# Kernel optimization log

Hardware: AMD Instinct MI355X
Metric: run time of the kernel (lower is better)

The kernel has to match this reference:

```python
import jax, jax.numpy as jnp
import numpy as np

N_HITS = 16384
N_EDGES = 262144
N_GROUPS = 512
N_EVENTS = 64
IN_CH = 25
HID = 128
HEADS = 4
DH = HID // HEADS
LAYERS = 3
EDGE_DIM = 5
FFN = 4 * HID
EPS = 1e-5


def setup_inputs() -> dict:
    key = jax.random.key(0)
    ks = jax.random.split(key, 16)
    def nrm(k, shape, s=0.05):
        return jax.random.normal(k, shape, dtype=jnp.float32) * s
    z = lambda *s: jnp.zeros(s, jnp.float32)
    return {
        "x": jax.random.normal(ks[0], (N_HITS, IN_CH), dtype=jnp.float32),
        "edge_index": jax.random.randint(ks[1], (2, N_EDGES), 0, N_HITS, dtype=jnp.int32),
        "edge_attr": jax.random.normal(ks[2], (N_EDGES, EDGE_DIM), dtype=jnp.float32),
        "group_indices": jax.random.randint(ks[3], (N_HITS,), 0, N_GROUPS, dtype=jnp.int32),
        "batch_indices_per_group": jnp.sort(jax.random.randint(ks[4], (N_GROUPS,), 0, N_EVENTS, dtype=jnp.int32)),
        "embed_W": nrm(ks[5], (IN_CH, HID)),
        "embed_b": z(HID),
        "blk_Wqkv": nrm(ks[6], (LAYERS, HID, 3 * HID)),
        "blk_bqkv": z(LAYERS, 3 * HID),
        "blk_We": nrm(ks[7], (LAYERS, EDGE_DIM, HID)),
        "blk_be": z(LAYERS, HID),
        "blk_Wo": nrm(ks[8], (LAYERS, HID, HID)),
        "blk_bo": z(LAYERS, HID),
        "ln1_g": jnp.ones((LAYERS, HID), jnp.float32),
        "ln1_b": z(LAYERS, HID),
        "ffn_W1": nrm(ks[9], (LAYERS, HID, FFN)),
        "ffn_b1": z(LAYERS, FFN),
        "ffn_W2": nrm(ks[10], (LAYERS, FFN, HID)),
        "ffn_b2": z(LAYERS, HID),
        "ln2_g": jnp.ones((LAYERS, HID), jnp.float32),
        "ln2_b": z(LAYERS, HID),
        "aff_W1": nrm(ks[11], (4 * HID, HID)),
        "aff_b1": z(HID),
        "aff_W2": nrm(ks[12], (HID, 1)),
        "aff_b2": z(1),
    }


def _layer_norm(v, g, b):
    mu = jnp.mean(v, axis=-1, keepdims=True)
    var = jnp.mean((v - mu) ** 2, axis=-1, keepdims=True)
    return (v - mu) * jax.lax.rsqrt(var + EPS) * g + b


def reference(x, edge_index, edge_attr, group_indices, batch_indices_per_group,
              embed_W, embed_b, blk_Wqkv, blk_bqkv, blk_We, blk_be, blk_Wo, blk_bo,
              ln1_g, ln1_b, ffn_W1, ffn_b1, ffn_W2, ffn_b2, ln2_g, ln2_b,
              aff_W1, aff_b1, aff_W2, aff_b2):
    n = x.shape[0]
    G = batch_indices_per_group.shape[0]
    src, dst = edge_index[0], edge_index[1]
    scale = 1.0 / np.sqrt(DH).astype(np.float32)

    h = x @ embed_W + embed_b  # [N, HID]
    for l in range(LAYERS):
        # edge-conditioned multi-head attention over the graph edges
        qkv = h @ blk_Wqkv[l] + blk_bqkv[l]
        q, k, v = jnp.split(qkv, 3, axis=-1)
        e = edge_attr @ blk_We[l] + blk_be[l]          # [E, HID]
        qe = q[dst].reshape(-1, HEADS, DH)              # [E, h, d]
        ke = (k[src] + e).reshape(-1, HEADS, DH)
        ve = (v[src] + e).reshape(-1, HEADS, DH)
        logits = jnp.einsum("ehd,ehd->eh", qe, ke) * scale
        m = jax.ops.segment_max(logits, dst, num_segments=n)
        m = jnp.where(jnp.isfinite(m), m, 0.0)          # nodes with no in-edges
        p = jnp.exp(logits - m[dst])
        s = jax.ops.segment_sum(p, dst, num_segments=n)
        attn = jax.ops.segment_sum(p[:, :, None] * ve, dst, num_segments=n)
        attn = (attn / jnp.maximum(s, 1e-9)[:, :, None]).reshape(n, HID)
        h = _layer_norm(h + attn @ blk_Wo[l] + blk_bo[l], ln1_g[l], ln1_b[l])
        f = jax.nn.relu(h @ ffn_W1[l] + ffn_b1[l]) @ ffn_W2[l] + ffn_b2[l]
        h = _layer_norm(h + f, ln2_g[l], ln2_b[l])

    # group pooling (multi-scatter)
    raw_view = x[:, 3].astype(jnp.int32)  # truncation, matches torch .long()
    cnt_all = jax.ops.segment_sum(jnp.ones((n,), jnp.float32), group_indices, num_segments=G)
    g_max = jax.ops.segment_max(h, group_indices, num_segments=G)
    g_max = jnp.where(cnt_all[:, None] > 0, g_max, 0.0)  # torch_scatter fills empty with 0

    def pool_view(view_id):
        w = (raw_view == view_id).astype(jnp.float32)
        cnt = jax.ops.segment_sum(w, group_indices, num_segments=G)
        summ = jax.ops.segment_sum(h * w[:, None], group_indices, num_segments=G)
        pooled = summ / jnp.maximum(cnt, 1.0)[:, None]
        has = (cnt > 0).astype(jnp.float32)[:, None]
        return pooled, has

    pool_x, has_x = pool_view(0)
    pool_y, has_y = pool_view(1)
    sum_feat = pool_x * has_x + pool_y * has_y
    valid = jnp.maximum(has_x + has_y, 1.0)
    ge = jnp.concatenate([sum_feat / valid, g_max], axis=1)  # [G, 2*HID]

    # pairwise affinity MLP: Linear(4H->H) split so the [G,G,4H] concat is never built
    W1a, W1b = aff_W1[: 2 * HID], aff_W1[2 * HID:]
    pre = (ge @ W1a)[:, None, :] + (ge @ W1b)[None, :, :] + aff_b1  # [G, G, HID]
    scores = (jax.nn.relu(pre) @ aff_W2 + aff_b2)[..., 0]           # [G, G]
    scores = 0.5 * (scores + scores.T)
    event_mask = batch_indices_per_group[:, None] == batch_indices_per_group[None, :]
    return jax.nn.sigmoid(scores) * event_mask.astype(scores.dtype)
```

## Files before the change

kernel.cpp:

```cpp
#include <hip/hip_runtime.h>
#include <hip/hip_bf16.h>

#define NHITS   16384
#define NEDGES  262144
#define NGROUPS 512
#define HID     128
#define LAYERS  3
#define FFND    512
#define MAXDEG  64
#define GCAP    96

typedef __attribute__((ext_vector_type(8))) short bf16x8;
typedef __attribute__((ext_vector_type(8))) unsigned short ushort8;
typedef __attribute__((ext_vector_type(4))) float floatx4;

__device__ __forceinline__ float bf2f(ushort u) {
    return __uint_as_float(((unsigned)u) << 16);
}
__device__ __forceinline__ ushort f2bf(float f) {
    unsigned u = __float_as_uint(f);
    unsigned r = (u + 0x7FFFu + ((u >> 16) & 1u)) >> 16;
    return (ushort)r;
}

__device__ __forceinline__ void gl2lds16(const ushort* gp, ushort* lp) {
    __builtin_amdgcn_global_load_lds(
        (const __attribute__((address_space(1))) unsigned int*)(gp),
        (__attribute__((address_space(3))) unsigned int*)(lp), 16, 0, 0);
}


struct TD { const float* src; ushort* dst; int K; int N; };
struct TDs { TD d[14]; };

__global__ __launch_bounds__(256) void transpose_all(TDs tds, int* __restrict__ zbuf,
                                                     int ztotal) {
    __shared__ float lds[32][33];
    if (blockIdx.y == 0) {
        for (int gz = blockIdx.x * 256 + threadIdx.x; gz < ztotal; gz += 64 * 256)
            zbuf[gz] = 0;
    }
    TD d = tds.d[blockIdx.y];
    int tX = d.N >> 5;
    int tiles = (d.K >> 5) * tX;
    if ((int)blockIdx.x >= tiles) return;
    int tk = blockIdx.x / tX, tn = blockIdx.x % tX;
    int k0 = tk * 32, n0 = tn * 32;
    int r = threadIdx.x >> 5, c = threadIdx.x & 31;
#pragma unroll
    for (int i = 0; i < 4; ++i)
        lds[r + i * 8][c] = d.src[(size_t)(k0 + r + i * 8) * d.N + n0 + c];
    __syncthreads();
#pragma unroll
    for (int i = 0; i < 4; ++i) {
        int n = n0 + r + i * 8;
        d.dst[(size_t)n * d.K + k0 + c] = f2bf(lds[c][r + i * 8]);
    }
}


__global__ __launch_bounds__(256) void scatter_embed(
        const int* __restrict__ src, const int* __restrict__ dst,
        const float* __restrict__ ea, const int* __restrict__ gidx,
        int* __restrict__ cnt, int* __restrict__ cnt2,
        int* __restrict__ ps, float* __restrict__ pea, int* __restrict__ hlist,
        const float* __restrict__ x, const float* __restrict__ embW,
        const float* __restrict__ embB, float* __restrict__ h,
        ushort* __restrict__ hb) {
    const int vb = blockIdx.x, t = threadIdx.x;
    if (vb < 1024) {
        int e = vb * 256 + t;
        int d = dst[e];
        int slot = atomicAdd(&cnt[d], 1);
        if (slot < MAXDEG) {
            size_t pos = (size_t)d * MAXDEG + slot;
            ps[pos] = src[e];
#pragma unroll
            for (int j = 0; j < 5; ++j) pea[pos * 5 + j] = ea[(size_t)e * 5 + j];
        }
        if (e < NHITS) {
            int g = gidx[e];
            int slot2 = atomicAdd(&cnt2[g], 1);
            if (slot2 < GCAP) hlist[g * GCAP + slot2] = e;
        }
    } else {
        __shared__ float xs[2][32];
        int base = (vb - 1024) * 32;
        for (int it = 0; it < 16; ++it) {
            int i0 = base + it * 2;
            __syncthreads();
            if (t < 25) xs[0][t] = x[(size_t)i0 * 25 + t];
            else if (t >= 128 && t < 153) xs[1][t - 128] = x[(size_t)(i0 + 1) * 25 + (t - 128)];
            __syncthreads();
            int node = i0 + (t >> 7), c = t & 127;
            const float* xr = xs[t >> 7];
            float s = embB[c];
#pragma unroll
            for (int k = 0; k < 25; ++k) s += xr[k] * embW[k * HID + c];
            h[(size_t)node * HID + c] = s;
            hb[(size_t)node * HID + c] = f2bf(s);
        }
    }
}


__global__ __launch_bounds__(256) void gemm_mfma_k(const ushort* __restrict__ A,
                                                   const ushort* __restrict__ Bt,
                                                   const float* __restrict__ bias,
                                                   ushort* __restrict__ C,
                                                   int N, int K, int relu) {
    __shared__ ushort As[128 * 32];
    __shared__ ushort Bs[128 * 32];
    const int t = threadIdx.x;
    const int lane = t & 63;
    const int w = t >> 6;
    const int wr = w >> 1, wc = w & 1;
    const int lm = lane & 15, q = lane >> 4;
    const int row0 = blockIdx.y * 128;
    const int col0 = blockIdx.x * 128;
    const int sr = t >> 2, sc = (t & 3) * 8;
    const int sr2 = (t + 256) >> 2, sc2 = ((t + 256) & 3) * 8;

    floatx4 acc[4][4] = {};
    for (int k0 = 0; k0 < K; k0 += 32) {
        gl2lds16(A + (size_t)(row0 + sr) * K + k0 + sc,   &As[t * 8]);
        gl2lds16(A + (size_t)(row0 + sr2) * K + k0 + sc2, &As[t * 8 + 2048]);
        gl2lds16(Bt + (size_t)(col0 + sr) * K + k0 + sc,   &Bs[t * 8]);
        gl2lds16(Bt + (size_t)(col0 + sr2) * K + k0 + sc2, &Bs[t * 8 + 2048]);
        __syncthreads();
        bf16x8 af[4], bf[4];
#pragma unroll
        for (int it = 0; it < 4; ++it)
            af[it] = *(const bf16x8*)&As[(wr * 64 + it * 16 + lm) * 32 + q * 8];
#pragma unroll
        for (int jt = 0; jt < 4; ++jt)
            bf[jt] = *(const bf16x8*)&Bs[(wc * 64 + jt * 16 + lm) * 32 + q * 8];
#pragma unroll
        for (int it = 0; it < 4; ++it)
#pragma unroll
            for (int jt = 0; jt < 4; ++jt)
                acc[it][jt] = __builtin_amdgcn_mfma_f32_16x16x32_bf16(
                    af[it], bf[jt], acc[it][jt], 0, 0, 0);
        __syncthreads();
    }
#pragma unroll
    for (int jt = 0; jt < 4; ++jt) {
        int col = col0 + wc * 64 + jt * 16 + lm;
        float bb = bias ? bias[col] : 0.f;
#pragma unroll
        for (int it = 0; it < 4; ++it)
#pragma unroll
            for (int r = 0; r < 4; ++r) {
                int row = row0 + wr * 64 + it * 16 + q * 4 + r;
                float o = acc[it][jt][r] + bb;
                if (relu) o = fmaxf(o, 0.f);
                C[(size_t)row * N + col] = f2bf(o);
            }
    }
}


__global__ __launch_bounds__(256) void gemm_qkv_k(const ushort* __restrict__ A,
                                                  const ushort* __restrict__ Bt,
                                                  const float* __restrict__ bias,
                                                  ushort* __restrict__ qb,
                                                  ushort* __restrict__ kvb,
                                                  int K) {
    __shared__ ushort As[128 * 32];
    __shared__ ushort Bs[128 * 32];
    const int t = threadIdx.x;
    const int lane = t & 63;
    const int w = t >> 6;
    const int wr = w >> 1, wc = w & 1;
    const int lm = lane & 15, q = lane >> 4;
    const int row0 = blockIdx.y * 128;
    const int col0 = blockIdx.x * 128;
    const int sr = t >> 2, sc = (t & 3) * 8;
    const int sr2 = (t + 256) >> 2, sc2 = ((t + 256) & 3) * 8;

    floatx4 acc[4][4] = {};
    for (int k0 = 0; k0 < K; k0 += 32) {
        gl2lds16(A + (size_t)(row0 + sr) * K + k0 + sc,   &As[t * 8]);
        gl2lds16(A + (size_t)(row0 + sr2) * K + k0 + sc2, &As[t * 8 + 2048]);
        gl2lds16(Bt + (size_t)(col0 + sr) * K + k0 + sc,   &Bs[t * 8]);
        gl2lds16(Bt + (size_t)(col0 + sr2) * K + k0 + sc2, &Bs[t * 8 + 2048]);
        __syncthreads();
        bf16x8 af[4], bf[4];
#pragma unroll
        for (int it = 0; it < 4; ++it)
            af[it] = *(const bf16x8*)&As[(wr * 64 + it * 16 + lm) * 32 + q * 8];
#pragma unroll
        for (int jt = 0; jt < 4; ++jt)
            bf[jt] = *(const bf16x8*)&Bs[(wc * 64 + jt * 16 + lm) * 32 + q * 8];
#pragma unroll
        for (int it = 0; it < 4; ++it)
#pragma unroll
            for (int jt = 0; jt < 4; ++jt)
                acc[it][jt] = __builtin_amdgcn_mfma_f32_16x16x32_bf16(
                    af[it], bf[jt], acc[it][jt], 0, 0, 0);
        __syncthreads();
    }
#pragma unroll
    for (int jt = 0; jt < 4; ++jt) {
        int col = col0 + wc * 64 + jt * 16 + lm;
        float bb = bias[col];
#pragma unroll
        for (int it = 0; it < 4; ++it)
#pragma unroll
            for (int r = 0; r < 4; ++r) {
                int row = row0 + wr * 64 + it * 16 + q * 4 + r;
                float o = acc[it][jt][r] + bb;
                ushort ob = f2bf(o);
                if (col < 128) qb[(size_t)row * 128 + col] = ob;
                else           kvb[(size_t)row * 256 + (col - 128)] = ob;
            }
    }
}


__global__ __launch_bounds__(256) void attn_kernel(const ushort* __restrict__ qb,
                                                   const ushort* __restrict__ kvb,
                                                   const int* __restrict__ ps,
                                                   const float* __restrict__ pea,
                                                   const int* __restrict__ cnt,
                                                   const float* __restrict__ We,
                                                   const float* __restrict__ be,
                                                   ushort* __restrict__ attnb) {
    __shared__ float WeS[640], beS[128];
    int t = threadIdx.x;
    for (int idx = t; idx < 640; idx += 256) WeS[idx] = We[idx];
    if (t < 128) beS[t] = be[t];
    __syncthreads();
    const int i = blockIdx.x * 4 + (t >> 6);
    const int lane = t & 63;
    const int grp = lane >> 4;
    const int cb = (lane & 15) * 8;
    float qv[8];
    {
        ushort8 qq = *(const ushort8*)(qb + (size_t)i * 128 + cb);
#pragma unroll
        for (int j = 0; j < 8; ++j) qv[j] = bf2f(qq[j]);
    }
    float pj[6];
#pragma unroll
    for (int k = 0; k < 5; ++k) {
        float s = 0.f;
#pragma unroll
        for (int j = 0; j < 8; ++j) s += qv[j] * WeS[k * 128 + cb + j];
        pj[k] = s;
    }
    {
        float sb = 0.f;
#pragma unroll
        for (int j = 0; j < 8; ++j) sb += qv[j] * beS[cb + j];
        pj[5] = sb;
    }
#pragma unroll
    for (int k = 0; k < 6; ++k) {
        pj[k] += __shfl_xor(pj[k], 1);
        pj[k] += __shfl_xor(pj[k], 2);
    }
    float S = 0.f, T0 = 0.f, T1 = 0.f, T2 = 0.f, T3 = 0.f, T4 = 0.f;
    float acc[8] = {};
    const int endc = min(cnt[i], MAXDEG);
    const size_t pbase = (size_t)i * MAXDEG;
    const float scale = 0.17677669529663687f;

#pragma unroll 4
    for (int p0 = 0; p0 < endc; p0 += 4) {
        int pp = p0 + grp;
        bool act = pp < endc;
        int slot = act ? pp : (endc - 1);
        int s = ps[pbase + slot];
        const float* eap = pea + (pbase + slot) * 5;
        float a0 = eap[0], a1 = eap[1], a2 = eap[2], a3 = eap[3], a4 = eap[4];
        const ushort* srow = kvb + (size_t)s * 256;
        ushort8 kk = *(const ushort8*)(srow + cb);
        ushort8 vv = *(const ushort8*)(srow + 128 + cb);
        float part = 0.f;
#pragma unroll
        for (int j = 0; j < 8; ++j) part += qv[j] * bf2f(kk[j]);
        part += __shfl_xor(part, 1);
        part += __shfl_xor(part, 2);
        float logit = (part + pj[5] + a0 * pj[0] + a1 * pj[1] + a2 * pj[2]
                       + a3 * pj[3] + a4 * pj[4]) * scale;
        float pe = act ? __expf(logit) : 0.f;
        S += pe;
        T0 += pe * a0; T1 += pe * a1; T2 += pe * a2; T3 += pe * a3; T4 += pe * a4;
#pragma unroll
        for (int j = 0; j < 8; ++j) acc[j] += pe * bf2f(vv[j]);
    }
#pragma unroll
    for (int j = 0; j < 8; ++j) {
        acc[j] += __shfl_xor(acc[j], 16);
        acc[j] += __shfl_xor(acc[j], 32);
    }
    S += __shfl_xor(S, 16);   S += __shfl_xor(S, 32);
    T0 += __shfl_xor(T0, 16); T0 += __shfl_xor(T0, 32);
    T1 += __shfl_xor(T1, 16); T1 += __shfl_xor(T1, 32);
    T2 += __shfl_xor(T2, 16); T2 += __shfl_xor(T2, 32);
    T3 += __shfl_xor(T3, 16); T3 += __shfl_xor(T3, 32);
    T4 += __shfl_xor(T4, 16); T4 += __shfl_xor(T4, 32);
    if (grp == 0) {
        float inv = 1.f / fmaxf(S, 1e-9f);
        ushort8 o;
#pragma unroll
        for (int j = 0; j < 8; ++j) {
            float wadd = WeS[cb + j] * T0 + WeS[128 + cb + j] * T1
                       + WeS[256 + cb + j] * T2 + WeS[384 + cb + j] * T3
                       + WeS[512 + cb + j] * T4 + beS[cb + j] * S;
            o[j] = f2bf((acc[j] + wadd) * inv);
        }
        *(ushort8*)(attnb + (size_t)i * HID + cb) = o;
    }
}


__global__ __launch_bounds__(256) void woffn_k(
        const ushort* __restrict__ attnb,
        const ushort* __restrict__ Wot, const float* __restrict__ bo,
        const float* __restrict__ ln1g, const float* __restrict__ ln1b,
        const ushort* __restrict__ W1t, const float* __restrict__ b1v,
        const ushort* __restrict__ W2t, const float* __restrict__ b2v,
        const float* __restrict__ ln2g, const float* __restrict__ ln2b,
        float* __restrict__ h, ushort* __restrict__ hb) {
    __shared__ ushort As[32 * 136];
    __shared__ ushort Bs[128 * 32];
    __shared__ ushort mid[32 * 520];
    __shared__ float redS[64], redQ[64];
    const int t = threadIdx.x;
    const int lane = t & 63;
    const int w = t >> 6;
    const int wr = w >> 1, wc = w & 1;
    const int lm = lane & 15, q = lane >> 4;
    const int row0 = blockIdx.x * 32;
    const int sr = t >> 2, sc = (t & 3) * 8;
    const int sr2 = (t + 256) >> 2, sc2 = ((t + 256) & 3) * 8;

    for (int i = t; i < 32 * 16; i += 256) {
        int row = i >> 4, c8 = (i & 15) * 8;
        *(ushort8*)&As[row * 136 + c8] =
            *(const ushort8*)(attnb + (size_t)(row0 + row) * HID + c8);
    }
    __syncthreads();

    floatx4 accW[4] = {};
    for (int k0 = 0; k0 < 128; k0 += 32) {
        gl2lds16(Wot + (size_t)sr * HID + k0 + sc,   &Bs[t * 8]);
        gl2lds16(Wot + (size_t)sr2 * HID + k0 + sc2, &Bs[t * 8 + 2048]);
        __syncthreads();
        bf16x8 af = *(const bf16x8*)&As[(wr * 16 + lm) * 136 + k0 + q * 8];
#pragma unroll
        for (int jt = 0; jt < 4; ++jt) {
            bf16x8 bf = *(const bf16x8*)&Bs[(wc * 64 + jt * 16 + lm) * 32 + q * 8];
            accW[jt] = __builtin_amdgcn_mfma_f32_16x16x32_bf16(af, bf, accW[jt], 0, 0, 0);
        }
        __syncthreads();
    }
    float o1[4][4];
    {
        float psum[4] = {}, psq[4] = {};
#pragma unroll
        for (int jt = 0; jt < 4; ++jt) {
            int col = wc * 64 + jt * 16 + lm;
            float bb = bo[col];
#pragma unroll
            for (int r = 0; r < 4; ++r) {
                int row = row0 + wr * 16 + q * 4 + r;
                float v = accW[jt][r] + bb + h[(size_t)row * HID + col];
                o1[jt][r] = v;
                psum[r] += v;
                psq[r] += v * v;
            }
        }
#pragma unroll
        for (int r = 0; r < 4; ++r) {
            float s = psum[r], ss = psq[r];
#pragma unroll
            for (int k = 1; k < 16; k <<= 1) {
                s += __shfl_xor(s, k, 16);
                ss += __shfl_xor(ss, k, 16);
            }
            psum[r] = s; psq[r] = ss;
        }
        if (lm == 0)
#pragma unroll
            for (int r = 0; r < 4; ++r) {
                int rl = wr * 16 + q * 4 + r;
                redS[rl * 2 + wc] = psum[r];
                redQ[rl * 2 + wc] = psq[r];
            }
        __syncthreads();
#pragma unroll
        for (int r = 0; r < 4; ++r) {
            int rl = wr * 16 + q * 4 + r;
            float tot = redS[rl * 2] + redS[rl * 2 + 1];
            float totq = redQ[rl * 2] + redQ[rl * 2 + 1];
            float mu = tot * (1.f / HID);
            float var = totq * (1.f / HID) - mu * mu;
            float rstd = rsqrtf(var + 1e-5f);
#pragma unroll
            for (int jt = 0; jt < 4; ++jt) {
                int col = wc * 64 + jt * 16 + lm;
                float o = (o1[jt][r] - mu) * rstd * ln1g[col] + ln1b[col];
                o1[jt][r] = o;
                As[(wr * 16 + q * 4 + r) * 136 + col] = f2bf(o);
            }
        }
    }
    __syncthreads();

    for (int nc = 0; nc < 4; ++nc) {
        floatx4 acc1[4] = {};
        for (int k0 = 0; k0 < 128; k0 += 32) {
            gl2lds16(W1t + (size_t)(nc * 128 + sr) * HID + k0 + sc,   &Bs[t * 8]);
            gl2lds16(W1t + (size_t)(nc * 128 + sr2) * HID + k0 + sc2, &Bs[t * 8 + 2048]);
            __syncthreads();
            bf16x8 af = *(const bf16x8*)&As[(wr * 16 + lm) * 136 + k0 + q * 8];
#pragma unroll
            for (int jt = 0; jt < 4; ++jt) {
                bf16x8 bf = *(const bf16x8*)&Bs[(wc * 64 + jt * 16 + lm) * 32 + q * 8];
                acc1[jt] = __builtin_amdgcn_mfma_f32_16x16x32_bf16(af, bf, acc1[jt], 0, 0, 0);
            }
            __syncthreads();
        }
#pragma unroll
        for (int jt = 0; jt < 4; ++jt) {
            int col = wc * 64 + jt * 16 + lm;
            float bb = b1v[nc * 128 + col];
#pragma unroll
            for (int r = 0; r < 4; ++r) {
                int row = wr * 16 + q * 4 + r;
                mid[row * 520 + nc * 128 + col] = f2bf(fmaxf(acc1[jt][r] + bb, 0.f));
            }
        }
    }
    __syncthreads();

    floatx4 acc2[4] = {};
    for (int k0 = 0; k0 < 512; k0 += 32) {
        gl2lds16(W2t + (size_t)sr * FFND + k0 + sc,   &Bs[t * 8]);
        gl2lds16(W2t + (size_t)sr2 * FFND + k0 + sc2, &Bs[t * 8 + 2048]);
        __syncthreads();
        bf16x8 af = *(const bf16x8*)&mid[(wr * 16 + lm) * 520 + k0 + q * 8];
#pragma unroll
        for (int jt = 0; jt < 4; ++jt) {
            bf16x8 bf = *(const bf16x8*)&Bs[(wc * 64 + jt * 16 + lm) * 32 + q * 8];
            acc2[jt] = __builtin_amdgcn_mfma_f32_16x16x32_bf16(af, bf, acc2[jt], 0, 0, 0);
        }
        __syncthreads();
    }
    float psum[4] = {}, psq[4] = {};
#pragma unroll
    for (int jt = 0; jt < 4; ++jt) {
        int col = wc * 64 + jt * 16 + lm;
        float bb = b2v[col];
#pragma unroll
        for (int r = 0; r < 4; ++r) {
            float v = acc2[jt][r] + bb + o1[jt][r];
            acc2[jt][r] = v;
            psum[r] += v;
            psq[r] += v * v;
        }
    }
#pragma unroll
    for (int r = 0; r < 4; ++r) {
        float s = psum[r], ss = psq[r];
#pragma unroll
        for (int k = 1; k < 16; k <<= 1) {
            s += __shfl_xor(s, k, 16);
            ss += __shfl_xor(ss, k, 16);
        }
        psum[r] = s; psq[r] = ss;
    }
    if (lm == 0)
#pragma unroll
        for (int r = 0; r < 4; ++r) {
            int rl = wr * 16 + q * 4 + r;
            redS[rl * 2 + wc] = psum[r];
            redQ[rl * 2 + wc] = psq[r];
        }
    __syncthreads();
#pragma unroll
    for (int r = 0; r < 4; ++r) {
        int rl = wr * 16 + q * 4 + r;
        float tot = redS[rl * 2] + redS[rl * 2 + 1];
        float totq = redQ[rl * 2] + redQ[rl * 2 + 1];
        float mu = tot * (1.f / HID);
        float var = totq * (1.f / HID) - mu * mu;
        float rstd = rsqrtf(var + 1e-5f);
        int row = row0 + rl;
#pragma unroll
        for (int jt = 0; jt < 4; ++jt) {
            int col = wc * 64 + jt * 16 + lm;
            float o = (acc2[jt][r] - mu) * rstd * ln2g[col] + ln2b[col];
            h[(size_t)row * HID + col] = o;
            hb[(size_t)row * HID + col] = f2bf(o);
        }
    }
}


__global__ __launch_bounds__(128) void pool_group(const float* __restrict__ h,
                                                  const float* __restrict__ x,
                                                  const int* __restrict__ hlist,
                                                  const int* __restrict__ cnt2,
                                                  ushort* __restrict__ geb) {
    int g = blockIdx.x, c = threadIdx.x;
    int n = min(cnt2[g], GCAP);
    float mx = -INFINITY, sx = 0.f, sy = 0.f, cx = 0.f, cy = 0.f;
    for (int p = 0; p < n; ++p) {
        int i = hlist[g * GCAP + p];
        float hv = h[(size_t)i * HID + c];
        mx = fmaxf(mx, hv);
        int view = (int)x[(size_t)i * 25 + 3];
        if (view == 0) { sx += hv; cx += 1.f; }
        else if (view == 1) { sy += hv; cy += 1.f; }
    }
    float gm = (n > 0) ? mx : 0.f;
    float px = sx / fmaxf(cx, 1.f), py = sy / fmaxf(cy, 1.f);
    float hx = cx > 0.f ? 1.f : 0.f, hy = cy > 0.f ? 1.f : 0.f;
    float sf = px * hx + py * hy;
    float valid = fmaxf(hx + hy, 1.f);
    geb[g * 256 + c] = f2bf(sf / valid);
    geb[g * 256 + 128 + c] = f2bf(gm);
}


__global__ __launch_bounds__(256) void score_final(const ushort* __restrict__ Cab,
                                                   const float* __restrict__ W2,
                                                   const float* __restrict__ b1v,
                                                   const float* __restrict__ b2,
                                                   const int* __restrict__ ev,
                                                   float* __restrict__ out) {
    int bi = blockIdx.y, bj = blockIdx.x;
    if (bj < bi) return;
    __shared__ float Ai[16][129], Bi[16][129], Aj[16][129], Bj[16][129];
    __shared__ float w2s[128], b1s[128];
    int t = threadIdx.y * 16 + threadIdx.x;
    int i0 = bi * 16, j0 = bj * 16;
    for (int idx = t; idx < 2048; idx += 256) {
        int r = idx >> 7, k = idx & 127;
        Ai[r][k] = bf2f(Cab[(size_t)(i0 + r) * 256 + k]);
        Bi[r][k] = bf2f(Cab[(size_t)(i0 + r) * 256 + 128 + k]);
        Aj[r][k] = bf2f(Cab[(size_t)(j0 + r) * 256 + k]);
        Bj[r][k] = bf2f(Cab[(size_t)(j0 + r) * 256 + 128 + k]);
    }
    if (t < 128) { w2s[t] = W2[t]; b1s[t] = b1v[t]; }
    __syncthreads();
    int tx = threadIdx.x, ty = threadIdx.y;
    float sij = 0.f, sji = 0.f;
#pragma unroll 4
    for (int k = 0; k < 128; ++k) {
        float pb = b1s[k], wk = w2s[k];
        sij += fmaxf(Ai[ty][k] + Bj[tx][k] + pb, 0.f) * wk;
        sji += fmaxf(Aj[tx][k] + Bi[ty][k] + pb, 0.f) * wk;
    }
    float z = 0.5f * (sij + sji) + b2[0];
    float sg = 1.f / (1.f + __expf(-z));
    int gi = i0 + ty, gj = j0 + tx;
    float res = (ev[gi] == ev[gj]) ? sg : 0.f;
    out[(size_t)gi * NGROUPS + gj] = res;
    out[(size_t)gj * NGROUPS + gi] = res;
}


static inline char* align256(char* p) {
    return (char*)(((uintptr_t)p + 255) & ~(uintptr_t)255);
}

extern "C" void kernel_launch(void* const* d_in, const int* in_sizes, int n_in,
                              void* d_out, int out_size, void* d_ws, size_t ws_size,
                              hipStream_t stream) {
    const float* x    = (const float*)d_in[0];
    const int* eidx   = (const int*)d_in[1];
    const float* ea   = (const float*)d_in[2];
    const int* gidx   = (const int*)d_in[3];
    const int* ev     = (const int*)d_in[4];
    const float* embW = (const float*)d_in[5];
    const float* embB = (const float*)d_in[6];
    const float* Wqkv = (const float*)d_in[7];
    const float* bqkv = (const float*)d_in[8];
    const float* We   = (const float*)d_in[9];
    const float* be   = (const float*)d_in[10];
    const float* Wo   = (const float*)d_in[11];
    const float* bo   = (const float*)d_in[12];
    const float* ln1g = (const float*)d_in[13];
    const float* ln1b = (const float*)d_in[14];
    const float* W1   = (const float*)d_in[15];
    const float* b1   = (const float*)d_in[16];
    const float* W2   = (const float*)d_in[17];
    const float* b2   = (const float*)d_in[18];
    const float* ln2g = (const float*)d_in[19];
    const float* ln2b = (const float*)d_in[20];
    const float* affW1 = (const float*)d_in[21];
    const float* affb1 = (const float*)d_in[22];
    const float* affW2 = (const float*)d_in[23];
    const float* affb2 = (const float*)d_in[24];

    const int* src = eidx;
    const int* dst = eidx + NEDGES;

    char* p = (char*)d_ws;
    float* h    = (float*)p;            p += (size_t)NHITS * HID * 4;
    float* pea  = (float*)p;            p += (size_t)NHITS * MAXDEG * 5 * 4;
    int* cnt    = (int*)p;              p += NHITS * 4;
    int* cnt2   = (int*)p;              p += NGROUPS * 4;
    int* ps     = (int*)p;              p += (size_t)NHITS * MAXDEG * 4;
    int* hlist  = (int*)p;              p += NGROUPS * GCAP * 4;
    p = align256(p);
    ushort* hb    = (ushort*)p;         p += (size_t)NHITS * HID * 2;
    ushort* qb    = (ushort*)p;         p += (size_t)NHITS * 128 * 2;
    ushort* kvb   = (ushort*)p;         p += (size_t)NHITS * 256 * 2;
    ushort* attnb = (ushort*)p;         p += (size_t)NHITS * HID * 2;
    ushort* geb   = (ushort*)p;         p += (size_t)NGROUPS * 256 * 2;
    ushort* Cab   = (ushort*)p;         p += (size_t)NGROUPS * 256 * 2;
    p = align256(p);
    ushort* Wqkvt = (ushort*)p;         p += (size_t)LAYERS * 384 * HID * 2;
    ushort* Wot   = (ushort*)p;         p += (size_t)LAYERS * HID * HID * 2;
    ushort* W1t   = (ushort*)p;         p += (size_t)LAYERS * FFND * HID * 2;
    ushort* W2t   = (ushort*)p;         p += (size_t)LAYERS * HID * FFND * 2;
    ushort* W1abt = (ushort*)p;         p += (size_t)256 * 256 * 2;

    TDs tds;
    for (int l = 0; l < LAYERS; ++l) {
        tds.d[l * 4 + 0] = { Wqkv + (size_t)l * HID * 384, Wqkvt + (size_t)l * 384 * HID, HID, 384 };
        tds.d[l * 4 + 1] = { Wo + (size_t)l * HID * HID,   Wot + (size_t)l * HID * HID,   HID, HID };
        tds.d[l * 4 + 2] = { W1 + (size_t)l * HID * FFND,  W1t + (size_t)l * FFND * HID,  HID, FFND };
        tds.d[l * 4 + 3] = { W2 + (size_t)l * FFND * HID,  W2t + (size_t)l * HID * FFND,  FFND, HID };
    }
    tds.d[12] = { affW1,             W1abt,             256, HID };
    tds.d[13] = { affW1 + 256 * HID, W1abt + 128 * 256, 256, HID };
    transpose_all<<<dim3(64, 14), 256, 0, stream>>>(tds, cnt, NHITS + NGROUPS);

    scatter_embed<<<1536, 256, 0, stream>>>(src, dst, ea, gidx, cnt, cnt2,
                                            ps, pea, hlist, x, embW, embB, h, hb);

    for (int l = 0; l < LAYERS; ++l) {
        gemm_qkv_k<<<dim3(3, NHITS / 128), 256, 0, stream>>>(
            hb, Wqkvt + (size_t)l * 384 * HID, bqkv + l * 384, qb, kvb, HID);
        attn_kernel<<<NHITS / 4, 256, 0, stream>>>(
            qb, kvb, ps, pea, cnt, We + (size_t)l * 5 * HID, be + l * HID, attnb);
        woffn_k<<<NHITS / 32, 256, 0, stream>>>(
            attnb, Wot + (size_t)l * HID * HID, bo + l * HID,
            ln1g + l * HID, ln1b + l * HID,
            W1t + (size_t)l * FFND * HID, b1 + l * FFND,
            W2t + (size_t)l * HID * FFND, b2 + l * HID,
            ln2g + l * HID, ln2b + l * HID, h, hb);
    }

    pool_group<<<NGROUPS, 128, 0, stream>>>(h, x, hlist, cnt2, geb);
    gemm_mfma_k<<<dim3(2, NGROUPS / 128), 256, 0, stream>>>(
        geb, W1abt, nullptr, Cab, 256, 256, 0);
    score_final<<<dim3(NGROUPS / 16, NGROUPS / 16), dim3(16, 16), 0, stream>>>(
        Cab, affW2, affb1, affb2, ev, (float*)d_out);
}
```

Baseline: 361.2 us.

## Fuse next-layer QKV projection into FFN kernel and pack edge data

The QKV projection for layers 2 and 3 now runs inside the Wo+FFN+LayerNorm kernel. It reuses the normalized bf16 rows already held in shared memory, which removes a separate GEMM launch and the hb write/read round trip. Edge source indices and attributes are packed into one 16-byte record per slot, with the attributes stored as bf16, so the attention kernel does a single vector load instead of six scattered loads. The trade-offs are lower precision on the edge attributes and extra serial MFMA work and register pressure in the already heavy FFN kernel.

```diff
diff --git a/kernel.cpp b/kernel.cpp
--- a/kernel.cpp
+++ b/kernel.cpp
@@ -63,7 +63,7 @@
         const int* __restrict__ src, const int* __restrict__ dst,
         const float* __restrict__ ea, const int* __restrict__ gidx,
         int* __restrict__ cnt, int* __restrict__ cnt2,
-        int* __restrict__ ps, float* __restrict__ pea, int* __restrict__ hlist,
+        int4* __restrict__ epk, int* __restrict__ hlist,
         const float* __restrict__ x, const float* __restrict__ embW,
         const float* __restrict__ embB, float* __restrict__ h,
         ushort* __restrict__ hb) {
@@ -73,10 +73,13 @@
         int d = dst[e];
         int slot = atomicAdd(&cnt[d], 1);
         if (slot < MAXDEG) {
-            size_t pos = (size_t)d * MAXDEG + slot;
-            ps[pos] = src[e];
-#pragma unroll
-            for (int j = 0; j < 5; ++j) pea[pos * 5 + j] = ea[(size_t)e * 5 + j];
+            const float* eap = ea + (size_t)e * 5;
+            int4 m;
+            m.x = src[e];
+            m.y = (int)((unsigned)f2bf(eap[0]) | ((unsigned)f2bf(eap[1]) << 16));
+            m.z = (int)((unsigned)f2bf(eap[2]) | ((unsigned)f2bf(eap[3]) << 16));
+            m.w = (int)(unsigned)f2bf(eap[4]);
+            epk[(size_t)d * MAXDEG + slot] = m;
         }
         if (e < NHITS) {
             int g = gidx[e];
@@ -209,8 +212,7 @@
 #pragma unroll
             for (int r = 0; r < 4; ++r) {
                 int row = row0 + wr * 64 + it * 16 + q * 4 + r;
-                float o = acc[it][jt][r] + bb;
-                ushort ob = f2bf(o);
+                ushort ob = f2bf(acc[it][jt][r] + bb);
                 if (col < 128) qb[(size_t)row * 128 + col] = ob;
                 else           kvb[(size_t)row * 256 + (col - 128)] = ob;
             }
@@ -220,8 +222,7 @@
 
 __global__ __launch_bounds__(256) void attn_kernel(const ushort* __restrict__ qb,
                                                    const ushort* __restrict__ kvb,
-                                                   const int* __restrict__ ps,
-                                                   const float* __restrict__ pea,
+                                                   const int4* __restrict__ epk,
                                                    const int* __restrict__ cnt,
                                                    const float* __restrict__ We,
                                                    const float* __restrict__ be,
@@ -271,9 +272,13 @@
         int pp = p0 + grp;
         bool act = pp < endc;
         int slot = act ? pp : (endc - 1);
-        int s = ps[pbase + slot];
-        const float* eap = pea + (pbase + slot) * 5;
-        float a0 = eap[0], a1 = eap[1], a2 = eap[2], a3 = eap[3], a4 = eap[4];
+        int4 m = epk[pbase + slot];
+        int s = m.x;
+        float a0 = bf2f((ushort)((unsigned)m.y & 0xffffu));
+        float a1 = bf2f((ushort)((unsigned)m.y >> 16));
+        float a2 = bf2f((ushort)((unsigned)m.z & 0xffffu));
+        float a3 = bf2f((ushort)((unsigned)m.z >> 16));
+        float a4 = bf2f((ushort)((unsigned)m.w & 0xffffu));
         const ushort* srow = kvb + (size_t)s * 256;
         ushort8 kk = *(const ushort8*)(srow + cb);
         ushort8 vv = *(const ushort8*)(srow + 128 + cb);
@@ -323,7 +328,9 @@
         const ushort* __restrict__ W1t, const float* __restrict__ b1v,
         const ushort* __restrict__ W2t, const float* __restrict__ b2v,
         const float* __restrict__ ln2g, const float* __restrict__ ln2b,
-        float* __restrict__ h, ushort* __restrict__ hb) {
+        float* __restrict__ h,
+        const ushort* __restrict__ Wqn, const float* __restrict__ bqn,
+        ushort* __restrict__ qb, ushort* __restrict__ kvb) {
     __shared__ ushort As[32 * 136];
     __shared__ ushort Bs[128 * 32];
     __shared__ ushort mid[32 * 520];
@@ -450,52 +457,85 @@
         }
         __syncthreads();
     }
-    float psum[4] = {}, psq[4] = {};
-#pragma unroll
-    for (int jt = 0; jt < 4; ++jt) {
-        int col = wc * 64 + jt * 16 + lm;
-        float bb = b2v[col];
+    {
+        float psum[4] = {}, psq[4] = {};
+#pragma unroll
+        for (int jt = 0; jt < 4; ++jt) {
+            int col = wc * 64 + jt * 16 + lm;
+            float bb = b2v[col];
+#pragma unroll
+            for (int r = 0; r < 4; ++r) {
+                float v = acc2[jt][r] + bb + o1[jt][r];
+                acc2[jt][r] = v;
+                psum[r] += v;
+                psq[r] += v * v;
+            }
+        }
 #pragma unroll
         for (int r = 0; r < 4; ++r) {
-            float v = acc2[jt][r] + bb + o1[jt][r];
-            acc2[jt][r] = v;
-            psum[r] += v;
-            psq[r] += v * v;
-        }
-    }
-#pragma unroll
-    for (int r = 0; r < 4; ++r) {
-        float s = psum[r], ss = psq[r];
-#pragma unroll
-        for (int k = 1; k < 16; k <<= 1) {
-            s += __shfl_xor(s, k, 16);
-            ss += __shfl_xor(ss, k, 16);
-        }
-        psum[r] = s; psq[r] = ss;
-    }
-    if (lm == 0)
+            float s = psum[r], ss = psq[r];
+#pragma unroll
+            for (int k = 1; k < 16; k <<= 1) {
+                s += __shfl_xor(s, k, 16);
+                ss += __shfl_xor(ss, k, 16);
+            }
+            psum[r] = s; psq[r] = ss;
+        }
+        if (lm == 0)
+#pragma unroll
+            for (int r = 0; r < 4; ++r) {
+                int rl = wr * 16 + q * 4 + r;
+                redS[rl * 2 + wc] = psum[r];
+                redQ[rl * 2 + wc] = psq[r];
+            }
+        __syncthreads();
 #pragma unroll
         for (int r = 0; r < 4; ++r) {
             int rl = wr * 16 + q * 4 + r;
-            redS[rl * 2 + wc] = psum[r];
-            redQ[rl * 2 + wc] = psq[r];
-        }
+            float tot = redS[rl * 2] + redS[rl * 2 + 1];
+            float totq = redQ[rl * 2] + redQ[rl * 2 + 1];
+            float mu = tot * (1.f / HID);
+            float var = totq * (1.f / HID) - mu * mu;
+            float rstd = rsqrtf(var + 1e-5f);
+            int row = row0 + rl;
+#pragma unroll
+            for (int jt = 0; jt < 4; ++jt) {
+                int col = wc * 64 + jt * 16 + lm;
+                float o = (acc2[jt][r] - mu) * rstd * ln2g[col] + ln2b[col];
+                h[(size_t)row * HID + col] = o;
+                if (Wqn) As[rl * 136 + col] = f2bf(o);
+            }
+        }
+    }
+    if (!Wqn) return;
     __syncthreads();
-#pragma unroll
-    for (int r = 0; r < 4; ++r) {
-        int rl = wr * 16 + q * 4 + r;
-        float tot = redS[rl * 2] + redS[rl * 2 + 1];
-        float totq = redQ[rl * 2] + redQ[rl * 2 + 1];
-        float mu = tot * (1.f / HID);
-        float var = totq * (1.f / HID) - mu * mu;
-        float rstd = rsqrtf(var + 1e-5f);
-        int row = row0 + rl;
+
+    for (int nc = 0; nc < 3; ++nc) {
+        floatx4 accq[4] = {};
+        for (int k0 = 0; k0 < 128; k0 += 32) {
+            gl2lds16(Wqn + (size_t)(nc * 128 + sr) * HID + k0 + sc,   &Bs[t * 8]);
+            gl2lds16(Wqn + (size_t)(nc * 128 + sr2) * HID + k0 + sc2, &Bs[t * 8 + 2048]);
+            __syncthreads();
+            bf16x8 af = *(const bf16x8*)&As[(wr * 16 + lm) * 136 + k0 + q * 8];
+#pragma unroll
+            for (int jt = 0; jt < 4; ++jt) {
+                bf16x8 bf = *(const bf16x8*)&Bs[(wc * 64 + jt * 16 + lm) * 32 + q * 8];
+                accq[jt] = __builtin_amdgcn_mfma_f32_16x16x32_bf16(af, bf, accq[jt], 0, 0, 0);
+            }
+            __syncthreads();
+        }
 #pragma unroll
         for (int jt = 0; jt < 4; ++jt) {
             int col = wc * 64 + jt * 16 + lm;
-            float o = (acc2[jt][r] - mu) * rstd * ln2g[col] + ln2b[col];
-            h[(size_t)row * HID + col] = o;
-            hb[(size_t)row * HID + col] = f2bf(o);
+            float bb = bqn[nc * 128 + col];
+#pragma unroll
+            for (int r = 0; r < 4; ++r) {
+                int row = row0 + wr * 16 + q * 4 + r;
+                ushort ob = f2bf(accq[jt][r] + bb);
+                if (nc == 0)      qb[(size_t)row * 128 + col] = ob;
+                else if (nc == 1) kvb[(size_t)row * 256 + col] = ob;
+                else              kvb[(size_t)row * 256 + 128 + col] = ob;
+            }
         }
     }
 }
@@ -603,12 +643,11 @@
 
     char* p = (char*)d_ws;
     float* h    = (float*)p;            p += (size_t)NHITS * HID * 4;
-    float* pea  = (float*)p;            p += (size_t)NHITS * MAXDEG * 5 * 4;
     int* cnt    = (int*)p;              p += NHITS * 4;
     int* cnt2   = (int*)p;              p += NGROUPS * 4;
-    int* ps     = (int*)p;              p += (size_t)NHITS * MAXDEG * 4;
     int* hlist  = (int*)p;              p += NGROUPS * GCAP * 4;
     p = align256(p);
+    int4* epk   = (int4*)p;             p += (size_t)NHITS * MAXDEG * 16;
     ushort* hb    = (ushort*)p;         p += (size_t)NHITS * HID * 2;
     ushort* qb    = (ushort*)p;         p += (size_t)NHITS * 128 * 2;
     ushort* kvb   = (ushort*)p;         p += (size_t)NHITS * 256 * 2;
@@ -634,19 +673,22 @@
     transpose_all<<<dim3(64, 14), 256, 0, stream>>>(tds, cnt, NHITS + NGROUPS);
 
     scatter_embed<<<1536, 256, 0, stream>>>(src, dst, ea, gidx, cnt, cnt2,
-                                            ps, pea, hlist, x, embW, embB, h, hb);
+                                            epk, hlist, x, embW, embB, h, hb);
+
+    gemm_qkv_k<<<dim3(3, NHITS / 128), 256, 0, stream>>>(
+        hb, Wqkvt, bqkv, qb, kvb, HID);
 
     for (int l = 0; l < LAYERS; ++l) {
-        gemm_qkv_k<<<dim3(3, NHITS / 128), 256, 0, stream>>>(
-            hb, Wqkvt + (size_t)l * 384 * HID, bqkv + l * 384, qb, kvb, HID);
         attn_kernel<<<NHITS / 4, 256, 0, stream>>>(
-            qb, kvb, ps, pea, cnt, We + (size_t)l * 5 * HID, be + l * HID, attnb);
+            qb, kvb, epk, cnt, We + (size_t)l * 5 * HID, be + l * HID, attnb);
+        const ushort* Wqn = (l + 1 < LAYERS) ? Wqkvt + (size_t)(l + 1) * 384 * HID : nullptr;
+        const float* bqn = (l + 1 < LAYERS) ? bqkv + (l + 1) * 384 : nullptr;
         woffn_k<<<NHITS / 32, 256, 0, stream>>>(
             attnb, Wot + (size_t)l * HID * HID, bo + l * HID,
             ln1g + l * HID, ln1b + l * HID,
             W1t + (size_t)l * FFND * HID, b1 + l * FFND,
             W2t + (size_t)l * HID * FFND, b2 + l * HID,
-            ln2g + l * HID, ln2b + l * HID, h, hb);
+            ln2g + l * HID, ln2b + l * HID, h, Wqn, bqn, qb, kvb);
     }
 
     pool_group<<<NGROUPS, 128, 0, stream>>>(h, x, hlist, cnt2, geb);
```

Result: no change. 357.0 us (-1.2%).
